# Kernel optimization log

Hardware: AMD Instinct MI355X
Metric: run time of the kernel (lower is better)

The kernel has to match this reference:

```python
import jax, jax.numpy as jnp
import numpy as np

HID = 256
EDGE_F = 64
N_CELL = 4096
N_EDGE = 65536
BSZ = 4
EPS = 1e-5


def setup_inputs() -> dict:
    key = jax.random.key(0)
    ks = jax.random.split(key, 12)
    def lin(k, fan_in, fan_out):
        # torch Linear default init: U(-1/sqrt(fan_in), 1/sqrt(fan_in))
        bound = 1.0 / np.sqrt(fan_in)
        kw, kb = jax.random.split(k)
        W = jax.random.uniform(kw, (fan_in, fan_out), jnp.float32, -bound, bound)
        b = jax.random.uniform(kb, (fan_out,), jnp.float32, -bound, bound)
        return W, b
    cell_x = jax.random.normal(ks[0], (BSZ, N_CELL, HID), jnp.float32)
    edge_index = jax.random.randint(ks[1], (BSZ, N_EDGE, 2), 0, N_CELL, jnp.int64)
    edge_attr = jax.random.normal(ks[2], (BSZ, N_EDGE, EDGE_F), jnp.float32)
    mW1, mb1 = lin(ks[3], HID + EDGE_F, HID)
    mW2, mb2 = lin(ks[4], HID, HID)
    uW1, ub1 = lin(ks[5], 2 * HID, HID)
    uW2, ub2 = lin(ks[6], HID, HID)
    gamma = jnp.ones((HID,), jnp.float32)
    beta = jnp.zeros((HID,), jnp.float32)
    return {"cell_x": cell_x, "edge_index": edge_index, "edge_attr": edge_attr,
            "mW1": mW1, "mb1": mb1, "mW2": mW2, "mb2": mb2,
            "uW1": uW1, "ub1": ub1, "uW2": uW2, "ub2": ub2,
            "gamma": gamma, "beta": beta}


def reference(cell_x, edge_index, edge_attr, mW1, mb1, mW2, mb2,
              uW1, ub1, uW2, ub2, gamma, beta):
    n_cell = cell_x.shape[1]
    src = jnp.clip(edge_index[..., 0], 0, n_cell - 1)  # [B, E]
    dst = jnp.clip(edge_index[..., 1], 0, n_cell - 1)  # [B, E]

    # gather source node features per edge: [B, E, H]
    src_x = jnp.take_along_axis(cell_x, src[..., None], axis=1)

    # edge message MLP
    m_in = jnp.concatenate([src_x, edge_attr], axis=-1)  # [B, E, H+F]
    msg = jax.nn.relu(m_in @ mW1 + mb1) @ mW2 + mb2      # [B, E, H]

    # mean aggregation at destination nodes (scatter-add + count)
    def agg_one(m, d):
        s = jax.ops.segment_sum(m, d, num_segments=n_cell)                    # [N, H]
        c = jax.ops.segment_sum(jnp.ones((d.shape[0],), m.dtype), d,
                                num_segments=n_cell)                          # [N]
        return s / jnp.maximum(c, 1.0)[:, None]
    agg = jax.vmap(agg_one)(msg, dst)  # [B, N, H]

    # node update MLP + residual LayerNorm
    u_in = jnp.concatenate([cell_x, agg], axis=-1)        # [B, N, 2H]
    out = jax.nn.relu(u_in @ uW1 + ub1) @ uW2 + ub2       # [B, N, H]
    h = cell_x + out
    mu = jnp.mean(h, axis=-1, keepdims=True)
    var = jnp.mean(jnp.square(h - mu), axis=-1, keepdims=True)
    return (h - mu) * jax.lax.rsqrt(var + EPS) * gamma + beta
```

## Files before the change

### kernel.cpp

```cpp
#include <hip/hip_runtime.h>
#include <hip/hip_bf16.h>

#define HID 256
#define EF  64
#define KIN 320
#define NC  4096
#define NE  65536
#define BSZ 4
#define EPSV 1e-5f

typedef unsigned short ushort_t;
typedef __attribute__((ext_vector_type(8))) short s16x8;
typedef __attribute__((ext_vector_type(16))) float f32x16;

#define EPAD 68
#define HPAD 260
#define UPAD 520
#define HSF  260

__device__ __forceinline__ ushort_t bf16_rne(float f) {
    unsigned u = __float_as_uint(f);
    return (ushort_t)((u + 0x7fffu + ((u >> 16) & 1u)) >> 16);
}
__device__ __forceinline__ float bf16_to_f(ushort_t u) {
    return __uint_as_float(((unsigned)u) << 16);
}
__device__ __forceinline__ unsigned pk_bf16(float a, float b) {
    __hip_bfloat162 h = __float22bfloat162_rn(make_float2(a, b));
    return *reinterpret_cast<unsigned*>(&h);
}
__device__ __forceinline__ void split_bf16(float v, ushort_t& h, ushort_t& l) {
    unsigned u = __float_as_uint(v);
    h = (ushort_t)(u >> 16);
    float hf = __uint_as_float(u & 0xffff0000u);
    l = (ushort_t)(__float_as_uint(v - hf) >> 16);
}

__device__ __forceinline__ void pack_one(const float* W, int idx,
                                         ushort_t* hi, ushort_t* lo) {
    int l = idx & 63;
    int tn = idx >> 6;
    int nt = tn & 7, t = tn >> 3;
    int k0 = t * 16 + (l >> 5) * 8;
    int col = nt * 32 + (l & 31);
    #pragma unroll
    for (int j = 0; j < 8; ++j) {
        float v = W[(size_t)(k0 + j) * 256 + col];
        ushort_t h, lw;
        split_bf16(v, h, lw);
        hi[(size_t)idx * 8 + j] = h;
        lo[(size_t)idx * 8 + j] = lw;
    }
}

#define FR1 10240
#define FR2 8192
#define PACK1B 104
#define FUSEB 256
#define ZEROB 256

__global__ __launch_bounds__(256)
void prep_kernel(const float* __restrict__ mW1, const float* __restrict__ uW1,
                 const float* __restrict__ uW2, const float* __restrict__ mW2,
                 const float* __restrict__ ub1, const float* __restrict__ mb2,
                 ushort_t* __restrict__ w1hi, ushort_t* __restrict__ w1lo,
                 ushort_t* __restrict__ u1hi, ushort_t* __restrict__ u1lo,
                 ushort_t* __restrict__ u2hi, ushort_t* __restrict__ u2lo,
                 float* __restrict__ W2u, float* __restrict__ bias2u,
                 float4* __restrict__ zp, int n4) {
    int bid = blockIdx.x;
    if (bid < PACK1B) {
        int idx = bid * 256 + threadIdx.x;
        if (idx < FR1) { pack_one(mW1, idx, w1hi, w1lo); return; }
        idx -= FR1;
        if (idx < FR2) { pack_one(uW1, idx, u1hi, u1lo); return; }
        idx -= FR2;
        pack_one(uW2, idx, u2hi, u2lo);
        return;
    }
    bid -= PACK1B;
    if (bid < FUSEB) {
        int k = bid, n = threadIdx.x;
        const float* wrow = mW2 + (size_t)k * 256;
        float acc = 0.f;
        #pragma unroll 8
        for (int m = 0; m < 256; ++m)
            acc = fmaf(wrow[m], uW1[(size_t)(256 + m) * 256 + n], acc);
        W2u[(size_t)k * 256 + n] = acc;
        return;
    }
    bid -= FUSEB;
    if (bid == 0) {
        int n = threadIdx.x;
        float acc = ub1[n];
        #pragma unroll 8
        for (int m = 0; m < 256; ++m)
            acc = fmaf(mb2[m], uW1[(size_t)(256 + m) * 256 + n], acc);
        bias2u[n] = acc;
        return;
    }
    bid -= 1;
    int i = bid * 256 + threadIdx.x;
    int stride = ZEROB * 256;
    float4 z = make_float4(0.f, 0.f, 0.f, 0.f);
    for (; i < n4; i += stride) zp[i] = z;
}

__global__ __launch_bounds__(512, 4)
void hp_kernel(const int* __restrict__ eidx, float* __restrict__ counts,
               const float* __restrict__ cell_x,
               const ushort_t* __restrict__ w1hi, const ushort_t* __restrict__ w1lo,
               const ushort_t* __restrict__ u1hi, const ushort_t* __restrict__ u1lo,
               float* __restrict__ Pe, ushort_t* __restrict__ Pn,
               const float* __restrict__ W2u,
               ushort_t* __restrict__ w2uhi, ushort_t* __restrict__ w2ulo) {
    __shared__ ushort_t Us[32 * HPAD];

    if (blockIdx.x < 512) {
        int i = blockIdx.x * 512 + threadIdx.x;
        int b = i >> 16;
        int2 v = ((const int2*)eidx)[i];
        int d = min(max(v.y, 0), NC - 1);
        atomicAdd(&counts[b * NC + d], 1.0f);
        return;
    }
    if (blockIdx.x >= 1024) {
        int idx = (blockIdx.x - 1024) * 512 + threadIdx.x;
        pack_one(W2u, idx, w2uhi, w2ulo);
        return;
    }

    const int tid = threadIdx.x;
    const size_t r0 = (size_t)(blockIdx.x - 512) * 32;
    const int wv = tid >> 6, ln = tid & 63;
    const int m32 = ln & 31, half = ln >> 5;
    const int col = wv * 32 + m32;

    const ushort_t* wph = w1hi + ((size_t)wv * 64 + ln) * 8;
    const ushort_t* wpl = w1lo + ((size_t)wv * 64 + ln) * 8;
    const ushort_t* uph = u1hi + ((size_t)wv * 64 + ln) * 8;
    const ushort_t* upl = u1lo + ((size_t)wv * 64 + ln) * 8;
    s16x8 wh = *(const s16x8*)wph, wl = *(const s16x8*)wpl;
    s16x8 uh = *(const s16x8*)uph, ul = *(const s16x8*)upl;

    {
        const int row = tid >> 4, c8 = tid & 15;
        const float4* crow = (const float4*)(cell_x + (r0 + row) * HID);
        #pragma unroll
        for (int i = 0; i < 4; ++i) {
            int c = c8 + i * 16;
            float4 v = crow[c];
            *(uint2*)&Us[row * HPAD + c * 4] =
                make_uint2(pk_bf16(v.x, v.y), pk_bf16(v.z, v.w));
        }
    }
    __syncthreads();

    f32x16 aw, au;
    #pragma unroll
    for (int r = 0; r < 16; ++r) { aw[r] = 0.f; au[r] = 0.f; }

    #pragma unroll 2
    for (int t = 0; t < 16; ++t) {
        int tn = (t + 1 < 16) ? t + 1 : 15;
        s16x8 whn = *(const s16x8*)(wph + (size_t)tn * 4096);
        s16x8 wln = *(const s16x8*)(wpl + (size_t)tn * 4096);
        s16x8 uhn = *(const s16x8*)(uph + (size_t)tn * 4096);
        s16x8 uln = *(const s16x8*)(upl + (size_t)tn * 4096);
        s16x8 a = *(const s16x8*)&Us[m32 * HPAD + t * 16 + half * 8];
        aw = __builtin_amdgcn_mfma_f32_32x32x16_bf16(a, wh, aw, 0, 0, 0);
        aw = __builtin_amdgcn_mfma_f32_32x32x16_bf16(a, wl, aw, 0, 0, 0);
        au = __builtin_amdgcn_mfma_f32_32x32x16_bf16(a, uh, au, 0, 0, 0);
        au = __builtin_amdgcn_mfma_f32_32x32x16_bf16(a, ul, au, 0, 0, 0);
        wh = whn; wl = wln; uh = uhn; ul = uln;
    }

    #pragma unroll
    for (int r = 0; r < 16; ++r) {
        int row = (r & 3) + 8 * (r >> 2) + 4 * half;
        Pe[(r0 + row) * 256 + col] = aw[r];
        Pn[(r0 + row) * 256 + col] = bf16_rne(au[r]);
    }
}

__global__ __launch_bounds__(512, 4)
void scansc_kernel(const int* __restrict__ eidx, const float* __restrict__ counts,
                   int* __restrict__ filled, int* __restrict__ sorted) {
    __shared__ int woffL[NC];
    __shared__ int wsum[8];

    const int t = threadIdx.x;
    const int b = blockIdx.x >> 7;

    int c[8];
    int ts = 0;
    const int base = b * NC + t * 8;
    #pragma unroll
    for (int j = 0; j < 8; ++j) { c[j] = (int)counts[base + j]; ts += c[j]; }

    int lane = t & 63;
    int x = ts;
    #pragma unroll
    for (int off = 1; off < 64; off <<= 1) {
        int y = __shfl_up(x, off, 64);
        if (lane >= off) x += y;
    }
    if (lane == 63) wsum[t >> 6] = x;
    __syncthreads();
    if (t == 0) {
        int s = 0;
        #pragma unroll
        for (int w = 0; w < 8; ++w) { int tmp = wsum[w]; wsum[w] = s; s += tmp; }
    }
    __syncthreads();
    int run = wsum[t >> 6] + (x - ts);
    #pragma unroll
    for (int j = 0; j < 8; ++j) { woffL[t * 8 + j] = run; run += c[j]; }
    __syncthreads();

    int e = (blockIdx.x & 127) * 512 + t;
    int2 v = ((const int2*)eidx)[(size_t)b * NE + e];
    int d = min(max(v.y, 0), NC - 1);
    int pos = woffL[d] + atomicAdd(&filled[b * NC + d], 1);
    sorted[(size_t)b * NE + pos] = e;
}

__global__ __launch_bounds__(512, 4)
void edge_kernel(const float* __restrict__ Pe,
                 const int*   __restrict__ eidx,
                 const int*   __restrict__ sorted,
                 const float* __restrict__ eattr,
                 const ushort_t* __restrict__ w1hi, const ushort_t* __restrict__ w1lo,
                 const float* __restrict__ b1,
                 float* __restrict__ aggf) {
    __shared__ ushort_t Xs[64 * EPAD];

    const int tid = threadIdx.x;
    const int b   = blockIdx.x >> 10;
    const int e0  = (blockIdx.x & 1023) * 64;
    const int wv = tid >> 6, ln = tid & 63;
    const int m32 = ln & 31, half = ln >> 5;
    const int col = wv * 32 + m32;

    int eid = sorted[(size_t)b * NE + e0 + ln];
    int2 ev = ((const int2*)eidx)[(size_t)b * NE + eid];
    int src = min(max(ev.x, 0), NC - 1);
    int dst = min(max(ev.y, 0), NC - 1);

    const ushort_t* ph = w1hi + ((size_t)(16 * 8 + wv) * 64 + ln) * 8;
    const ushort_t* pl = w1lo + ((size_t)(16 * 8 + wv) * 64 + ln) * 8;
    s16x8 bh0 = *(const s16x8*)ph;
    s16x8 bl0 = *(const s16x8*)pl;
    s16x8 bh1 = *(const s16x8*)(ph + 4096);
    s16x8 bl1 = *(const s16x8*)(pl + 4096);
    s16x8 bh2 = *(const s16x8*)(ph + 8192);
    s16x8 bl2 = *(const s16x8*)(pl + 8192);
    s16x8 bh3 = *(const s16x8*)(ph + 12288);
    s16x8 bl3 = *(const s16x8*)(pl + 12288);

    float t0[16], t1[16];
    {
        const float* pb = Pe + (size_t)b * NC * 256 + col;
        #pragma unroll
        for (int r = 0; r < 16; ++r) {
            int rw = (r & 3) + 8 * (r >> 2) + 4 * half;
            t0[r] = pb[(size_t)__shfl(src, rw, 64) * 256];
            t1[r] = pb[(size_t)__shfl(src, rw + 32, 64) * 256];
        }
    }

    {
        const int rowE = tid >> 3, c8 = tid & 7;
        int eidr = __shfl(eid, rowE, 64);
        const float4* arow = (const float4*)(eattr + ((size_t)b * NE + eidr) * EF);
        #pragma unroll
        for (int i = 0; i < 2; ++i) {
            int c = c8 + i * 8;
            float4 v = arow[c];
            *(uint2*)&Xs[rowE * EPAD + c * 4] =
                make_uint2(pk_bf16(v.x, v.y), pk_bf16(v.z, v.w));
        }
    }
    __syncthreads();

    f32x16 A0, A1;
    {
        float bias = b1[col];
        #pragma unroll
        for (int r = 0; r < 16; ++r) { A0[r] = bias; A1[r] = bias; }
    }
    {
        int ao = m32 * EPAD + half * 8;
        s16x8 a0, a1;
        a0 = *(const s16x8*)&Xs[ao];      a1 = *(const s16x8*)&Xs[ao + 32 * EPAD];
        A0 = __builtin_amdgcn_mfma_f32_32x32x16_bf16(a0, bh0, A0, 0, 0, 0);
        A0 = __builtin_amdgcn_mfma_f32_32x32x16_bf16(a0, bl0, A0, 0, 0, 0);
        A1 = __builtin_amdgcn_mfma_f32_32x32x16_bf16(a1, bh0, A1, 0, 0, 0);
        A1 = __builtin_amdgcn_mfma_f32_32x32x16_bf16(a1, bl0, A1, 0, 0, 0);
        a0 = *(const s16x8*)&Xs[ao + 16]; a1 = *(const s16x8*)&Xs[ao + 16 + 32 * EPAD];
        A0 = __builtin_amdgcn_mfma_f32_32x32x16_bf16(a0, bh1, A0, 0, 0, 0);
        A0 = __builtin_amdgcn_mfma_f32_32x32x16_bf16(a0, bl1, A0, 0, 0, 0);
        A1 = __builtin_amdgcn_mfma_f32_32x32x16_bf16(a1, bh1, A1, 0, 0, 0);
        A1 = __builtin_amdgcn_mfma_f32_32x32x16_bf16(a1, bl1, A1, 0, 0, 0);
        a0 = *(const s16x8*)&Xs[ao + 32]; a1 = *(const s16x8*)&Xs[ao + 32 + 32 * EPAD];
        A0 = __builtin_amdgcn_mfma_f32_32x32x16_bf16(a0, bh2, A0, 0, 0, 0);
        A0 = __builtin_amdgcn_mfma_f32_32x32x16_bf16(a0, bl2, A0, 0, 0, 0);
        A1 = __builtin_amdgcn_mfma_f32_32x32x16_bf16(a1, bh2, A1, 0, 0, 0);
        A1 = __builtin_amdgcn_mfma_f32_32x32x16_bf16(a1, bl2, A1, 0, 0, 0);
        a0 = *(const s16x8*)&Xs[ao + 48]; a1 = *(const s16x8*)&Xs[ao + 48 + 32 * EPAD];
        A0 = __builtin_amdgcn_mfma_f32_32x32x16_bf16(a0, bh3, A0, 0, 0, 0);
        A0 = __builtin_amdgcn_mfma_f32_32x32x16_bf16(a0, bl3, A0, 0, 0, 0);
        A1 = __builtin_amdgcn_mfma_f32_32x32x16_bf16(a1, bh3, A1, 0, 0, 0);
        A1 = __builtin_amdgcn_mfma_f32_32x32x16_bf16(a1, bl3, A1, 0, 0, 0);
    }

    #pragma unroll
    for (int r = 0; r < 16; ++r) {
        A0[r] = fmaxf(A0[r] + t0[r], 0.f);
        A1[r] = fmaxf(A1[r] + t1[r], 0.f);
    }

    {
        const int l31 = ln & 31;
        int dl = __shfl(dst, l31, 64);
        int dp = __shfl(dst, (l31 == 0) ? 0 : l31 - 1, 64);
        if (l31 == 0) dp = ~dl;
        unsigned m = (unsigned)__ballot(dl != dp);
        unsigned rem = m & ~1u;
        int lo = 0;
        while (lo < 32) {
            int hi = rem ? (int)__builtin_ctz(rem) : 32;
            rem &= rem - 1;
            int d = __shfl(dl, lo, 64);
            float s = 0.f;
            #pragma unroll
            for (int r = 0; r < 16; ++r) {
                int row = (r & 3) + 8 * (r >> 2) + 4 * half;
                s += (row >= lo && row < hi) ? A0[r] : 0.f;
            }
            s += __shfl_xor(s, 32, 64);
            if (ln < 32) atomicAdd(&aggf[((size_t)b * NC + d) * HID + col], s);
            lo = hi;
        }
        dl = __shfl(dst, 32 + l31, 64);
        dp = __shfl(dst, 32 + ((l31 == 0) ? 0 : l31 - 1), 64);
        if (l31 == 0) dp = ~dl;
        m = (unsigned)__ballot(dl != dp);
        rem = m & ~1u;
        lo = 0;
        while (lo < 32) {
            int hi = rem ? (int)__builtin_ctz(rem) : 32;
            rem &= rem - 1;
            int d = __shfl(dl, lo, 64);
            float s = 0.f;
            #pragma unroll
            for (int r = 0; r < 16; ++r) {
                int row = (r & 3) + 8 * (r >> 2) + 4 * half;
                s += (row >= lo && row < hi) ? A1[r] : 0.f;
            }
            s += __shfl_xor(s, 32, 64);
            if (ln < 32) atomicAdd(&aggf[((size_t)b * NC + d) * HID + col], s);
            lo = hi;
        }
    }
}

__global__ __launch_bounds__(512, 6)
void node_kernel(const float* __restrict__ cell_x,
                 const float* __restrict__ aggf,
                 const float* __restrict__ counts,
                 const ushort_t* __restrict__ Pn,
                 const ushort_t* __restrict__ w2uhi, const ushort_t* __restrict__ w2ulo,
                 const float* __restrict__ bias2u,
                 const ushort_t* __restrict__ u2hi, const ushort_t* __restrict__ u2lo,
                 const float* __restrict__ b2,
                 const float* __restrict__ gamma, const float* __restrict__ beta,
                 float* __restrict__ out) {
    __shared__ ushort_t Us[32 * UPAD];
    float* hs = (float*)Us;

    const int tid = threadIdx.x;
    const int b   = blockIdx.x >> 7;
    const int r0  = (blockIdx.x & 127) * 32;
    const int wv = tid >> 6, ln = tid & 63;
    const int m32 = ln & 31, half = ln >> 5;
    const int col = wv * 32 + m32;

    const ushort_t* b1ph = w2uhi + ((size_t)wv * 64 + ln) * 8;
    const ushort_t* b1pl = w2ulo + ((size_t)wv * 64 + ln) * 8;
    s16x8 bhi = *(const s16x8*)b1ph;
    s16x8 blo = *(const s16x8*)b1pl;

    ushort_t pnt[16];
    {
        const ushort_t* pb = Pn + ((size_t)b * NC + r0) * 256 + col;
        #pragma unroll
        for (int r = 0; r < 16; ++r) {
            int row = (r & 3) + 8 * (r >> 2) + 4 * half;
            pnt[r] = pb[(size_t)row * 256];
        }
    }

    {
        const int row = tid >> 4, c8 = tid & 15;
        float inv = 1.0f / fmaxf(counts[b * NC + r0 + row], 1.0f);
        const float4* grow = (const float4*)(aggf + ((size_t)b * NC + r0 + row) * HID);
        #pragma unroll
        for (int i = 0; i < 4; ++i) {
            int c = c8 + i * 16;
            float4 g = grow[c];
            *(uint2*)&Us[row * HPAD + c * 4] =
                make_uint2(pk_bf16(g.x * inv, g.y * inv), pk_bf16(g.z * inv, g.w * inv));
        }
    }
    __syncthreads();

    f32x16 acc;
    {
        float bias = bias2u[col];
        #pragma unroll
        for (int r = 0; r < 16; ++r) acc[r] = bias;
    }
    #pragma unroll 2
    for (int t = 0; t < 16; ++t) {
        int tn1 = (t + 1 < 16) ? t + 1 : 15;
        s16x8 bhin = *(const s16x8*)(b1ph + (size_t)tn1 * 4096);
        s16x8 blon = *(const s16x8*)(b1pl + (size_t)tn1 * 4096);
        s16x8 a = *(const s16x8*)&Us[m32 * HPAD + t * 16 + half * 8];
        acc = __builtin_amdgcn_mfma_f32_32x32x16_bf16(a, bhi, acc, 0, 0, 0);
        acc = __builtin_amdgcn_mfma_f32_32x32x16_bf16(a, blo, acc, 0, 0, 0);
        bhi = bhin; blo = blon;
    }

    #pragma unroll
    for (int r = 0; r < 16; ++r) acc[r] += bf16_to_f(pnt[r]);

    const ushort_t* b2ph = u2hi + ((size_t)wv * 64 + ln) * 8;
    const ushort_t* b2pl = u2lo + ((size_t)wv * 64 + ln) * 8;
    bhi = *(const s16x8*)b2ph;
    blo = *(const s16x8*)b2pl;

    __syncthreads();

    #pragma unroll
    for (int r = 0; r < 16; ++r) {
        int row = (r & 3) + 8 * (r >> 2) + 4 * half;
        Us[row * HPAD + col] = bf16_rne(fmaxf(acc[r], 0.f));
    }
    __syncthreads();

    float cxt[16];
    #pragma unroll
    for (int r = 0; r < 16; ++r) {
        int row = (r & 3) + 8 * (r >> 2) + 4 * half;
        cxt[r] = cell_x[((size_t)b * NC + r0 + row) * HID + col];
    }

    f32x16 c2;
    {
        float bias = b2[col];
        #pragma unroll
        for (int r = 0; r < 16; ++r) c2[r] = bias;
    }
    #pragma unroll 2
    for (int t = 0; t < 16; ++t) {
        int tn1 = (t + 1 < 16) ? t + 1 : 15;
        s16x8 bhin = *(const s16x8*)(b2ph + (size_t)tn1 * 4096);
        s16x8 blon = *(const s16x8*)(b2pl + (size_t)tn1 * 4096);
        s16x8 a = *(const s16x8*)&Us[m32 * HPAD + t * 16 + half * 8];
        c2 = __builtin_amdgcn_mfma_f32_32x32x16_bf16(a, bhi, c2, 0, 0, 0);
        c2 = __builtin_amdgcn_mfma_f32_32x32x16_bf16(a, blo, c2, 0, 0, 0);
        bhi = bhin; blo = blon;
    }
    __syncthreads();

    #pragma unroll
    for (int r = 0; r < 16; ++r) {
        int row = (r & 3) + 8 * (r >> 2) + 4 * half;
        hs[row * HSF + col] = c2[r] + cxt[r];
    }
    __syncthreads();

    #pragma unroll
    for (int i = 0; i < 4; ++i) {
        int r = wv * 4 + i;
        float v[4];
        float s = 0.f, q = 0.f;
        #pragma unroll
        for (int j = 0; j < 4; ++j) {
            v[j] = hs[r * HSF + ln + 64 * j];
            s += v[j];
            q = fmaf(v[j], v[j], q);
        }
        #pragma unroll
        for (int off = 32; off > 0; off >>= 1) {
            s += __shfl_xor(s, off, 64);
            q += __shfl_xor(q, off, 64);
        }
        float mu = s * (1.0f / HID);
        float var = q * (1.0f / HID) - mu * mu;
        float rs = rsqrtf(var + EPSV);
        float* orow = out + ((size_t)b * NC + r0 + r) * HID;
        #pragma unroll
        for (int j = 0; j < 4; ++j) {
            int c = ln + 64 * j;
            orow[c] = (v[j] - mu) * rs * gamma[c] + beta[c];
        }
    }
}

extern "C" void kernel_launch(void* const* d_in, const int* in_sizes, int n_in,
                              void* d_out, int out_size, void* d_ws, size_t ws_size,
                              hipStream_t stream) {
    const float* cell_x = (const float*)d_in[0];
    const int*   eidx   = (const int*)d_in[1];
    const float* eattr  = (const float*)d_in[2];
    const float* mW1    = (const float*)d_in[3];
    const float* mb1    = (const float*)d_in[4];
    const float* mW2    = (const float*)d_in[5];
    const float* mb2    = (const float*)d_in[6];
    const float* uW1    = (const float*)d_in[7];
    const float* ub1    = (const float*)d_in[8];
    const float* uW2    = (const float*)d_in[9];
    const float* ub2    = (const float*)d_in[10];
    const float* gamma  = (const float*)d_in[11];
    const float* beta   = (const float*)d_in[12];
    float* out = (float*)d_out;

    float* aggf   = (float*)d_ws;
    float* counts = aggf + (size_t)BSZ * NC * HID;
    int*   filled = (int*)(counts + BSZ * NC);
    int*   sorted = filled + BSZ * NC;
    ushort_t* w1hi = (ushort_t*)(sorted + (size_t)BSZ * NE);
    ushort_t* w1lo = w1hi + KIN * HID;
    ushort_t* u1hi = w1lo + KIN * HID;
    ushort_t* u1lo = u1hi + HID * HID;
    ushort_t* u2hi = u1lo + HID * HID;
    ushort_t* u2lo = u2hi + HID * HID;
    ushort_t* w2uhi = u2lo + HID * HID;
    ushort_t* w2ulo = w2uhi + HID * HID;
    float*    W2u   = (float*)(w2ulo + HID * HID);
    float*    bias2u = W2u + HID * HID;
    float*    Pe   = bias2u + HID;
    ushort_t* Pn   = (ushort_t*)(Pe + (size_t)BSZ * NC * 256);

    int n4 = (BSZ * NC * HID * 4 + BSZ * NC * 4 + BSZ * NC * 4) / 16;
    prep_kernel<<<PACK1B + FUSEB + 1 + ZEROB, 256, 0, stream>>>(
        mW1, uW1, uW2, mW2, ub1, mb2,
        w1hi, w1lo, u1hi, u1lo, u2hi, u2lo, W2u, bias2u, (float4*)d_ws, n4);
    hp_kernel<<<1040, 512, 0, stream>>>(eidx, counts, cell_x,
                                        w1hi, w1lo, u1hi, u1lo, Pe, Pn,
                                        W2u, w2uhi, w2ulo);
    scansc_kernel<<<512, 512, 0, stream>>>(eidx, counts, filled, sorted);
    edge_kernel<<<BSZ * NE / 64, 512, 0, stream>>>(Pe, eidx, sorted, eattr,
                                                   w1hi, w1lo, mb1, aggf);
    node_kernel<<<BSZ * NC / 32, 512, 0, stream>>>(cell_x, aggf, counts, Pn,
                                                   w2uhi, w2ulo, bias2u,
                                                   u2hi, u2lo, ub2,
                                                   gamma, beta, out);
}
```

Baseline: 255.5 us.

## Halve node rows per block and use suffix-sum segmented reduction in edge scatter

The hp and node kernels now process 16 node rows per block instead of 32, doubling the block count for more parallelism across CUs. The MFMA tiles still compute 32 rows, so half of the matrix work is redundant and its results are masked out. In the edge kernel, the per-segment masked sums are replaced by a running suffix-sum difference, which cuts the number of predicated adds per segment. The node kernel's launch bounds occupancy hint is lowered from 6 to 4.

```diff
diff --git a/kernel.cpp b/kernel.cpp
--- a/kernel.cpp
+++ b/kernel.cpp
@@ -124,14 +124,14 @@
         atomicAdd(&counts[b * NC + d], 1.0f);
         return;
     }
-    if (blockIdx.x >= 1024) {
-        int idx = (blockIdx.x - 1024) * 512 + threadIdx.x;
+    if (blockIdx.x >= 1536) {
+        int idx = (blockIdx.x - 1536) * 512 + threadIdx.x;
         pack_one(W2u, idx, w2uhi, w2ulo);
         return;
     }
 
     const int tid = threadIdx.x;
-    const size_t r0 = (size_t)(blockIdx.x - 512) * 32;
+    const size_t r0 = (size_t)(blockIdx.x - 512) * 16;
     const int wv = tid >> 6, ln = tid & 63;
     const int m32 = ln & 31, half = ln >> 5;
     const int col = wv * 32 + m32;
@@ -144,11 +144,11 @@
     s16x8 uh = *(const s16x8*)uph, ul = *(const s16x8*)upl;
 
     {
-        const int row = tid >> 4, c8 = tid & 15;
+        const int row = tid >> 5, c8 = tid & 31;
         const float4* crow = (const float4*)(cell_x + (r0 + row) * HID);
         #pragma unroll
-        for (int i = 0; i < 4; ++i) {
-            int c = c8 + i * 16;
+        for (int i = 0; i < 2; ++i) {
+            int c = c8 + i * 32;
             float4 v = crow[c];
             *(uint2*)&Us[row * HPAD + c * 4] =
                 make_uint2(pk_bf16(v.x, v.y), pk_bf16(v.z, v.w));
@@ -178,8 +178,10 @@
     #pragma unroll
     for (int r = 0; r < 16; ++r) {
         int row = (r & 3) + 8 * (r >> 2) + 4 * half;
-        Pe[(r0 + row) * 256 + col] = aw[r];
-        Pn[(r0 + row) * 256 + col] = bf16_rne(au[r]);
+        if (row < 16) {
+            Pe[(r0 + row) * 256 + col] = aw[r];
+            Pn[(r0 + row) * 256 + col] = bf16_rne(au[r]);
+        }
     }
 }
 
@@ -327,17 +329,23 @@
         if (l31 == 0) dp = ~dl;
         unsigned m = (unsigned)__ballot(dl != dp);
         unsigned rem = m & ~1u;
+        float prev = (((A0[0] + A0[1]) + (A0[2] + A0[3])) + ((A0[4] + A0[5]) + (A0[6] + A0[7])))
+                   + (((A0[8] + A0[9]) + (A0[10] + A0[11])) + ((A0[12] + A0[13]) + (A0[14] + A0[15])));
         int lo = 0;
         while (lo < 32) {
             int hi = rem ? (int)__builtin_ctz(rem) : 32;
             rem &= rem - 1;
             int d = __shfl(dl, lo, 64);
-            float s = 0.f;
-            #pragma unroll
-            for (int r = 0; r < 16; ++r) {
-                int row = (r & 3) + 8 * (r >> 2) + 4 * half;
-                s += (row >= lo && row < hi) ? A0[r] : 0.f;
+            float shi = 0.f;
+            if (hi < 32) {
+                #pragma unroll
+                for (int r = 0; r < 16; ++r) {
+                    int row = (r & 3) + 8 * (r >> 2) + 4 * half;
+                    shi += (row >= hi) ? A0[r] : 0.f;
+                }
             }
+            float s = prev - shi;
+            prev = shi;
             s += __shfl_xor(s, 32, 64);
             if (ln < 32) atomicAdd(&aggf[((size_t)b * NC + d) * HID + col], s);
             lo = hi;
@@ -347,17 +355,23 @@
         if (l31 == 0) dp = ~dl;
         m = (unsigned)__ballot(dl != dp);
         rem = m & ~1u;
+        prev = (((A1[0] + A1[1]) + (A1[2] + A1[3])) + ((A1[4] + A1[5]) + (A1[6] + A1[7])))
+             + (((A1[8] + A1[9]) + (A1[10] + A1[11])) + ((A1[12] + A1[13]) + (A1[14] + A1[15])));
         lo = 0;
         while (lo < 32) {
             int hi = rem ? (int)__builtin_ctz(rem) : 32;
             rem &= rem - 1;
             int d = __shfl(dl, lo, 64);
-            float s = 0.f;
-            #pragma unroll
-            for (int r = 0; r < 16; ++r) {
-                int row = (r & 3) + 8 * (r >> 2) + 4 * half;
-                s += (row >= lo && row < hi) ? A1[r] : 0.f;
+            float shi = 0.f;
+            if (hi < 32) {
+                #pragma unroll
+                for (int r = 0; r < 16; ++r) {
+                    int row = (r & 3) + 8 * (r >> 2) + 4 * half;
+                    shi += (row >= hi) ? A1[r] : 0.f;
+                }
             }
+            float s = prev - shi;
+            prev = shi;
             s += __shfl_xor(s, 32, 64);
             if (ln < 32) atomicAdd(&aggf[((size_t)b * NC + d) * HID + col], s);
             lo = hi;
@@ -365,7 +379,7 @@
     }
 }
 
-__global__ __launch_bounds__(512, 6)
+__global__ __launch_bounds__(512, 4)
 void node_kernel(const float* __restrict__ cell_x,
                  const float* __restrict__ aggf,
                  const float* __restrict__ counts,
@@ -380,8 +394,8 @@
     float* hs = (float*)Us;
 
     const int tid = threadIdx.x;
-    const int b   = blockIdx.x >> 7;
-    const int r0  = (blockIdx.x & 127) * 32;
+    const int b   = blockIdx.x >> 8;
+    const int r0  = (blockIdx.x & 255) * 16;
     const int wv = tid >> 6, ln = tid & 63;
     const int m32 = ln & 31, half = ln >> 5;
     const int col = wv * 32 + m32;
@@ -396,18 +410,18 @@
         const ushort_t* pb = Pn + ((size_t)b * NC + r0) * 256 + col;
         #pragma unroll
         for (int r = 0; r < 16; ++r) {
-            int row = (r & 3) + 8 * (r >> 2) + 4 * half;
+            int row = ((r & 3) + 8 * (r >> 2) + 4 * half) & 15;
             pnt[r] = pb[(size_t)row * 256];
         }
     }
 
     {
-        const int row = tid >> 4, c8 = tid & 15;
+        const int row = tid >> 5, c8 = tid & 31;
         float inv = 1.0f / fmaxf(counts[b * NC + r0 + row], 1.0f);
         const float4* grow = (const float4*)(aggf + ((size_t)b * NC + r0 + row) * HID);
         #pragma unroll
-        for (int i = 0; i < 4; ++i) {
-            int c = c8 + i * 16;
+        for (int i = 0; i < 2; ++i) {
+            int c = c8 + i * 32;
             float4 g = grow[c];
             *(uint2*)&Us[row * HPAD + c * 4] =
                 make_uint2(pk_bf16(g.x * inv, g.y * inv), pk_bf16(g.z * inv, g.w * inv));
@@ -445,14 +459,14 @@
     #pragma unroll
     for (int r = 0; r < 16; ++r) {
         int row = (r & 3) + 8 * (r >> 2) + 4 * half;
-        Us[row * HPAD + col] = bf16_rne(fmaxf(acc[r], 0.f));
+        if (row < 16) Us[row * HPAD + col] = bf16_rne(fmaxf(acc[r], 0.f));
     }
     __syncthreads();
 
     float cxt[16];
     #pragma unroll
     for (int r = 0; r < 16; ++r) {
-        int row = (r & 3) + 8 * (r >> 2) + 4 * half;
+        int row = ((r & 3) + 8 * (r >> 2) + 4 * half) & 15;
         cxt[r] = cell_x[((size_t)b * NC + r0 + row) * HID + col];
     }
 
@@ -477,13 +491,13 @@
     #pragma unroll
     for (int r = 0; r < 16; ++r) {
         int row = (r & 3) + 8 * (r >> 2) + 4 * half;
-        hs[row * HSF + col] = c2[r] + cxt[r];
-    }
-    __syncthreads();
-
-    #pragma unroll
-    for (int i = 0; i < 4; ++i) {
-        int r = wv * 4 + i;
+        if (row < 16) hs[row * HSF + col] = c2[r] + cxt[r];
+    }
+    __syncthreads();
+
+    #pragma unroll
+    for (int i = 0; i < 2; ++i) {
+        int r = wv * 2 + i;
         float v[4];
         float s = 0.f, q = 0.f;
         #pragma unroll
@@ -548,13 +562,13 @@
     prep_kernel<<<PACK1B + FUSEB + 1 + ZEROB, 256, 0, stream>>>(
         mW1, uW1, uW2, mW2, ub1, mb2,
         w1hi, w1lo, u1hi, u1lo, u2hi, u2lo, W2u, bias2u, (float4*)d_ws, n4);
-    hp_kernel<<<1040, 512, 0, stream>>>(eidx, counts, cell_x,
+    hp_kernel<<<1552, 512, 0, stream>>>(eidx, counts, cell_x,
                                         w1hi, w1lo, u1hi, u1lo, Pe, Pn,
                                         W2u, w2uhi, w2ulo);
     scansc_kernel<<<512, 512, 0, stream>>>(eidx, counts, filled, sorted);
     edge_kernel<<<BSZ * NE / 64, 512, 0, stream>>>(Pe, eidx, sorted, eattr,
                                                    w1hi, w1lo, mb1, aggf);
-    node_kernel<<<BSZ * NC / 32, 512, 0, stream>>>(cell_x, aggf, counts, Pn,
+    node_kernel<<<BSZ * NC / 16, 512, 0, stream>>>(cell_x, aggf, counts, Pn,
                                                    w2uhi, w2ulo, bias2u,
                                                    u2hi, u2lo, ub2,
                                                    gamma, beta, out);
```

New measurement: 263.4 us. +3.1%, slower.
